# Kernel optimization log

Hardware: AMD Instinct MI355X
Metric: run time of the kernel (lower is better)

The kernel has to match this reference:

```python
import jax, jax.numpy as jnp
import numpy as np
from jax import lax

B, T, F, D, K = 64, 1000, 140, 256, 7
TAU, V_TH, EPS, ALPHA = 2.0, 1.0, 1e-5, 2.0
PAD = (K - 1) // 2

# Heaviside spike with ATan surrogate gradient (spikingjelly default, alpha=2)
@jax.custom_vjp
def spike_fn(x):
    return (x >= 0.0).astype(x.dtype)

def _spike_fwd(x):
    return spike_fn(x), x

def _spike_bwd(x, g):
    sg = (ALPHA / 2.0) / (1.0 + (jnp.pi / 2.0 * ALPHA * x) ** 2)
    return (g * sg,)

spike_fn.defvjp(_spike_fwd, _spike_bwd)

def lif(x_seq):
    """Multi-step LIF: v += (x - v)/tau, hard reset to 0 on spike. x_seq: (T,B,D)."""
    def step(v, x):
        v = v + (x - v) / TAU
        s = spike_fn(v - V_TH)
        return v * (1.0 - s), s
    _, spikes = lax.scan(step, jnp.zeros_like(x_seq[0]), x_seq)
    return spikes

def bn(x, g, b, m, v):
    # eval-mode BatchNorm1d over channel dim D (last axis of (T,B,D))
    return (x - m) * (g * lax.rsqrt(v + EPS)) + b

def setup_inputs() -> dict:
    key = jax.random.key(0)
    ks = jax.random.split(key, 4)
    s = 0.05
    return {
        "x": jax.random.normal(ks[0], (B, T, F), jnp.float32),
        "pw_w": jax.random.normal(ks[1], (D, F), jnp.float32) * s,
        "pw_b": jnp.zeros((D,), jnp.float32),
        "dw_w": jax.random.normal(ks[2], (D, 1, K), jnp.float32) * s,  # depthwise (O,I/g,K)
        "bn1_g": jnp.ones((D,), jnp.float32),
        "bn1_b": jnp.zeros((D,), jnp.float32),
        "bn1_m": jnp.zeros((D,), jnp.float32),
        "bn1_v": jnp.ones((D,), jnp.float32),
        "lin_w": jax.random.normal(ks[3], (D, D), jnp.float32) * s,
        "bn2_g": jnp.ones((D,), jnp.float32),
        "bn2_b": jnp.zeros((D,), jnp.float32),
        "bn2_m": jnp.zeros((D,), jnp.float32),
        "bn2_v": jnp.ones((D,), jnp.float32),
    }

def reference(x, pw_w, pw_b, dw_w, bn1_g, bn1_b, bn1_m, bn1_v,
              lin_w, bn2_g, bn2_b, bn2_m, bn2_v):
    # pointwise conv: (B,T,F) -> (B,D,T)
    h = jnp.einsum('btf,df->bdt', x, pw_w) + pw_b[None, :, None]
    # depthwise temporal conv, groups=D, same padding
    h = lax.conv_general_dilated(h, dw_w, window_strides=(1,),
                                 padding=[(PAD, PAD)], feature_group_count=D,
                                 dimension_numbers=('NCH', 'OIH', 'NCH'))
    h = jnp.transpose(h, (2, 0, 1))  # (T,B,D) multi-step layout
    h = lif(bn(h, bn1_g, bn1_b, bn1_m, bn1_v))
    residual = h
    h = jnp.einsum('tbd,ed->tbe', h, lin_w)
    h = lif(bn(h, bn2_g, bn2_b, bn2_m, bn2_v))
    return h + residual
```

## Files before the change

kernel.cpp:

```cpp
#include <hip/hip_runtime.h>
#include <hip/hip_bf16.h>

#define B_  64
#define T_  1000
#define F_  140
#define D_  256
#define EPS_ 1e-5f

#define W2_ 16

#define CL_ 50
#define NC_ 20

#define CWR_ 42
#define NCH_ 24
#define HST_ 268
#define AST_ 168

typedef __attribute__((ext_vector_type(8))) short bf16x8;
typedef __attribute__((ext_vector_type(4))) short bf16x4;
typedef __attribute__((ext_vector_type(4))) float f32x4;
typedef unsigned long long u64;

static __device__ inline short f2bf(float f) {
  __hip_bfloat16 h = __float2bfloat16(f);
  return *reinterpret_cast<short*>(&h);
}
static __device__ inline float bf2f(short s) {
  unsigned int u = ((unsigned int)(unsigned short)s) << 16;
  return __uint_as_float(u);
}

__global__ __launch_bounds__(256) void k0_prep(const float* __restrict__ lw,
                                               float* __restrict__ lwT,
                                               const float* __restrict__ pw,
                                               short* __restrict__ wfrag) {
  int i = blockIdx.x * 256 + threadIdx.x;
  if (i < 65536) {
    int e = i >> 8, d = i & 255;
    lwT[(size_t)d * D_ + e] = lw[(size_t)e * D_ + d];
  } else if (i < 65536 + 40960) {
    int j = i - 65536;
    int q = j & 7;
    int lane = (j >> 3) & 63;
    int rest = j >> 9;
    int kk = rest % 5, ntile = rest / 5;
    int n = ntile * 16 + (lane & 15);
    int k = kk * 32 + (lane >> 4) * 8 + q;
    wfrag[j] = (k < F_) ? f2bf(pw[(size_t)n * F_ + k]) : (short)0;
  }
}

__global__ __launch_bounds__(256, 4) void k12_fused(const float* __restrict__ x,
                                                    const short* __restrict__ wfrag,
                                                    const float* __restrict__ bias,
                                                    const float* __restrict__ dww,
                                                    const float* __restrict__ g1,
                                                    const float* __restrict__ b1,
                                                    const float* __restrict__ m1,
                                                    const float* __restrict__ v1,
                                                    u64* __restrict__ bits) {
  __shared__ short smem[64 * HST_];
  short* Abuf = smem;
  short* hbuf = smem;
  const int b = blockIdx.x;
  const int c = blockIdx.y;
  const int tb = CWR_ * c - 19;
  const int tid = threadIdx.x;
  const int lane = tid & 63, wv = tid >> 6;
  const int lr = lane & 15, quad = lane >> 4;

  {
    const int arow = tid >> 2, aseg = tid & 3;
    const int ak0 = aseg * 36;
    const int anum4 = (aseg == 3) ? 8 : 9;
    const int ta = tb + arow;
    short* adst = Abuf + arow * AST_ + ak0;
    if (ta >= 0 && ta < T_) {
      const float* xrow = x + ((size_t)b * T_ + ta) * F_ + ak0;
#pragma unroll
      for (int q = 0; q < 9; q++) {
        if (q < anum4) {
          float4 av = *(const float4*)(xrow + q * 4);
          bf16x4 pk = {f2bf(av.x), f2bf(av.y), f2bf(av.z), f2bf(av.w)};
          *(bf16x4*)(adst + q * 4) = pk;
        }
      }
    } else {
      bf16x4 z = {0, 0, 0, 0};
#pragma unroll
      for (int q = 0; q < 9; q++)
        if (q < anum4) *(bf16x4*)(adst + q * 4) = z;
    }
    if (aseg == 3) {
      bf16x4 z = {0, 0, 0, 0};
#pragma unroll
      for (int q = 0; q < 5; q++) *(bf16x4*)(adst + 32 + q * 4) = z;
    }
  }

  const short* wfb = wfrag + (size_t)(wv * 4 * 5) * 512 + lane * 8;
  bf16x8 bfr[4];
#pragma unroll
  for (int j = 0; j < 4; j++)
    bfr[j] = *(const bf16x8*)(wfb + (size_t)(j * 5 + 0) * 512);
  __syncthreads();

  f32x4 acc[4][4] = {};
#pragma unroll
  for (int kk = 0; kk < 5; kk++) {
    bf16x8 bnext[4];
    if (kk < 4) {
#pragma unroll
      for (int j = 0; j < 4; j++)
        bnext[j] = *(const bf16x8*)(wfb + (size_t)(j * 5 + kk + 1) * 512);
    }
    bf16x8 af[4];
#pragma unroll
    for (int i = 0; i < 4; i++)
      af[i] = *(const bf16x8*)(Abuf + (i * 16 + lr) * AST_ + kk * 32 + quad * 8);
#pragma unroll
    for (int i = 0; i < 4; i++)
#pragma unroll
      for (int j = 0; j < 4; j++)
        acc[i][j] = __builtin_amdgcn_mfma_f32_16x16x32_bf16(af[i], bfr[j], acc[i][j], 0, 0, 0);
    if (kk < 4) {
#pragma unroll
      for (int j = 0; j < 4; j++) bfr[j] = bnext[j];
    }
  }
  __syncthreads();

#pragma unroll
  for (int j = 0; j < 4; j++) {
    const int n = wv * 64 + j * 16 + lr;
    const float badd = bias[n];
#pragma unroll
    for (int i = 0; i < 4; i++) {
#pragma unroll
      for (int r = 0; r < 4; r++) {
        const int row = i * 16 + quad * 4 + r;
        const int t = tb + row;
        short val = (t >= 0 && t < T_) ? f2bf(acc[i][j][r] + badd) : (short)0;
        hbuf[row * HST_ + n] = val;
      }
    }
  }
  __syncthreads();

  {
    const int d = tid;
    const float scv = g1[d] * rsqrtf(v1[d] + EPS_);
    float w2[7];
#pragma unroll
    for (int k = 0; k < 7; k++) w2[k] = dww[d * 7 + k] * (0.5f * scv);
    const float sh2 = 0.5f * (b1[d] - m1[d] * scv);

    float win0 = bf2f(hbuf[0 * HST_ + d]);
    float win1 = bf2f(hbuf[1 * HST_ + d]);
    float win2 = bf2f(hbuf[2 * HST_ + d]);
    float win3 = bf2f(hbuf[3 * HST_ + d]);
    float win4 = bf2f(hbuf[4 * HST_ + d]);
    float win5 = bf2f(hbuf[5 * HST_ + d]);
    float v = 0.f;
    u64 mymask = 0;

#pragma unroll
    for (int s0 = 0; s0 < 56; s0 += 8) {
      float tap[8];
#pragma unroll
      for (int g = 0; g < 8; g++) tap[g] = bf2f(hbuf[(s0 + g + 6) * HST_ + d]);
#pragma unroll
      for (int g = 0; g < 8; g++) {
        const int s = s0 + g;
        float u2 = win0 * w2[0] + win1 * w2[1] + win2 * w2[2] + win3 * w2[3] +
                   win4 * w2[4] + win5 * w2[5] + tap[g] * w2[6] + sh2;
        v = 0.5f * v + u2;
        bool sp = (v >= 1.0f);
        if (s >= W2_) {
          u64 mask = __ballot(sp);
          if (lane == (s - W2_)) mymask = mask;
        }
        v = sp ? 0.f : v;
        win0 = win1; win1 = win2; win2 = win3; win3 = win4; win4 = win5; win5 = tap[g];
      }
    }
    {
      float tap[2];
#pragma unroll
      for (int g = 0; g < 2; g++) tap[g] = bf2f(hbuf[(56 + g + 6) * HST_ + d]);
#pragma unroll
      for (int g = 0; g < 2; g++) {
        const int s = 56 + g;
        float u2 = win0 * w2[0] + win1 * w2[1] + win2 * w2[2] + win3 * w2[3] +
                   win4 * w2[4] + win5 * w2[5] + tap[g] * w2[6] + sh2;
        v = 0.5f * v + u2;
        bool sp = (v >= 1.0f);
        u64 mask = __ballot(sp);
        if (lane == (s - W2_)) mymask = mask;
        v = sp ? 0.f : v;
        win0 = win1; win1 = win2; win2 = win3; win3 = win4; win4 = win5; win5 = tap[g];
      }
    }
    const int tw0 = CWR_ * c;
    if (lane < CWR_) {
      const int t = tw0 + lane;
      if (t < T_)
        bits[((size_t)b * 4 + wv) * T_ + t] = mymask;
    }
  }
}

__global__ __launch_bounds__(256) void k3_lin_lif(const u64* __restrict__ bits,
                                                  const float* __restrict__ lwT,
                                                  const float* __restrict__ g2,
                                                  const float* __restrict__ b2,
                                                  const float* __restrict__ m2,
                                                  const float* __restrict__ v2,
                                                  float* __restrict__ out) {
  __shared__ u64 sb[4 * 80];
  const int b = blockIdx.x;
  const int t0 = blockIdx.y * CL_;
  const int tstart = (t0 >= W2_) ? t0 - W2_ : 0;
  const int nwarm = t0 - tstart;
  const int nsteps = nwarm + CL_;
  const int e = threadIdx.x;
  {
    const int dq = e >> 6, sidx = e & 63;
    const u64* src = bits + ((size_t)b * 4 + dq) * T_ + tstart;
    if (sidx < nsteps) sb[dq * 80 + sidx] = src[sidx];
    const int s2 = sidx + 64;
    if (s2 < nsteps) sb[dq * 80 + s2] = src[s2];
  }
  __syncthreads();

  const float sc = g2[e] * rsqrtf(v2[e] + EPS_);
  const float shf = b2[e] - m2[e] * sc;
  const int eq = e >> 6, eb = e & 63;
  float v = 0.f;

  if (nwarm) {
#pragma unroll
    for (int s0 = 0; s0 < W2_; s0 += 4) {
      u64 a0[4], a1[4], a2[4], a3[4];
#pragma unroll
      for (int g = 0; g < 4; g++) {
        a0[g] = sb[0 * 80 + s0 + g]; a1[g] = sb[1 * 80 + s0 + g];
        a2[g] = sb[2 * 80 + s0 + g]; a3[g] = sb[3 * 80 + s0 + g];
      }
#pragma unroll
      for (int g = 0; g < 4; g++) {
        float u = shf;
        if (a0[g] | a1[g] | a2[g] | a3[g]) {
          float acc = 0.f;
          u64 mm;
          mm = a0[g]; while (mm) { int l = __builtin_ctzll(mm); mm &= mm - 1; acc += lwT[(size_t)(l) * D_ + e]; }
          mm = a1[g]; while (mm) { int l = __builtin_ctzll(mm); mm &= mm - 1; acc += lwT[(size_t)(64 + l) * D_ + e]; }
          mm = a2[g]; while (mm) { int l = __builtin_ctzll(mm); mm &= mm - 1; acc += lwT[(size_t)(128 + l) * D_ + e]; }
          mm = a3[g]; while (mm) { int l = __builtin_ctzll(mm); mm &= mm - 1; acc += lwT[(size_t)(192 + l) * D_ + e]; }
          u = acc * sc + shf;
        }
        v = 0.5f * (v + u);
        v = (v >= 1.0f) ? 0.f : v;
      }
    }
  }
  float* op = out + ((size_t)t0 * B_ + b) * D_ + e;
  const size_t ts = (size_t)B_ * D_;
#pragma unroll
  for (int s0 = 0; s0 < CL_; s0 += 5) {
    u64 a0[5], a1[5], a2[5], a3[5];
#pragma unroll
    for (int g = 0; g < 5; g++) {
      const int s = nwarm + s0 + g;
      a0[g] = sb[0 * 80 + s]; a1[g] = sb[1 * 80 + s];
      a2[g] = sb[2 * 80 + s]; a3[g] = sb[3 * 80 + s];
    }
#pragma unroll
    for (int g = 0; g < 5; g++) {
      float u = shf;
      if (a0[g] | a1[g] | a2[g] | a3[g]) {
        float acc = 0.f;
        u64 mm;
        mm = a0[g]; while (mm) { int l = __builtin_ctzll(mm); mm &= mm - 1; acc += lwT[(size_t)(l) * D_ + e]; }
        mm = a1[g]; while (mm) { int l = __builtin_ctzll(mm); mm &= mm - 1; acc += lwT[(size_t)(64 + l) * D_ + e]; }
        mm = a2[g]; while (mm) { int l = __builtin_ctzll(mm); mm &= mm - 1; acc += lwT[(size_t)(128 + l) * D_ + e]; }
        mm = a3[g]; while (mm) { int l = __builtin_ctzll(mm); mm &= mm - 1; acc += lwT[(size_t)(192 + l) * D_ + e]; }
        u = acc * sc + shf;
      }
      v = 0.5f * (v + u);
      bool sp = (v >= 1.0f);
      u64 myw = (eq == 0) ? a0[g] : (eq == 1) ? a1[g] : (eq == 2) ? a2[g] : a3[g];
      float s1 = (float)((myw >> eb) & 1ull);
      op[(size_t)(s0 + g) * ts] = (sp ? 1.0f : 0.0f) + s1;
      v = sp ? 0.f : v;
    }
  }
}

extern "C" void kernel_launch(void* const* d_in, const int* in_sizes, int n_in,
                              void* d_out, int out_size, void* d_ws, size_t ws_size,
                              hipStream_t stream) {
  const float* x    = (const float*)d_in[0];
  const float* pw_w = (const float*)d_in[1];
  const float* pw_b = (const float*)d_in[2];
  const float* dw_w = (const float*)d_in[3];
  const float* g1   = (const float*)d_in[4];
  const float* b1   = (const float*)d_in[5];
  const float* m1   = (const float*)d_in[6];
  const float* v1   = (const float*)d_in[7];
  const float* lw   = (const float*)d_in[8];
  const float* g2   = (const float*)d_in[9];
  const float* b2   = (const float*)d_in[10];
  const float* m2   = (const float*)d_in[11];
  const float* v2   = (const float*)d_in[12];
  float* out = (float*)d_out;

  char* ws = (char*)d_ws;
  u64* bits = (u64*)ws;
  float* lwT = (float*)(ws + 2048000);
  short* wfrag = (short*)(ws + 2048000 + 262144);

  k0_prep<<<(65536 + 40960 + 255) / 256, 256, 0, stream>>>(lw, lwT, pw_w, wfrag);
  dim3 g_k12(B_, NCH_);
  k12_fused<<<g_k12, 256, 0, stream>>>(x, wfrag, pw_b, dw_w, g1, b1, m1, v1, bits);
  dim3 g_k3(B_, NC_);
  k3_lin_lif<<<g_k3, 256, 0, stream>>>(bits, lwT, g2, b2, m2, v2, out);
}
```

Before: 156.2 us.

## Fuse sparse linear+LIF2 stage into conv/LIF1 kernel via shared-memory spike masks

Merges the second-stage kernel (sparse spike-driven linear, BN2, LIF2, residual output) into the first fused kernel. Spike ballot masks for all 58 steps of each chunk, warm-up included, are kept in shared memory rather than written to a global bit buffer and re-read. The second LIF is warmed up over the 16 overlap steps already present in each chunk. This removes one kernel launch and the global round trip of the spike bits. In exchange the fused kernel's blocks run longer and have more register and shared-memory pressure, and the time-chunking of stage two now follows the 42-step conv chunks.

```diff
diff --git a/kernel.cpp b/kernel.cpp
--- a/kernel.cpp
+++ b/kernel.cpp
@@ -7,13 +7,9 @@
 #define D_  256
 #define EPS_ 1e-5f
 
-#define W2_ 16
-
-#define CL_ 50
-#define NC_ 20
-
 #define CWR_ 42
 #define NCH_ 24
+#define W1_  16
 #define HST_ 268
 #define AST_ 168
 
@@ -51,16 +47,22 @@
   }
 }
 
-__global__ __launch_bounds__(256, 4) void k12_fused(const float* __restrict__ x,
-                                                    const short* __restrict__ wfrag,
-                                                    const float* __restrict__ bias,
-                                                    const float* __restrict__ dww,
-                                                    const float* __restrict__ g1,
-                                                    const float* __restrict__ b1,
-                                                    const float* __restrict__ m1,
-                                                    const float* __restrict__ v1,
-                                                    u64* __restrict__ bits) {
+__global__ __launch_bounds__(256, 4) void k123_fused(const float* __restrict__ x,
+                                                     const short* __restrict__ wfrag,
+                                                     const float* __restrict__ bias,
+                                                     const float* __restrict__ dww,
+                                                     const float* __restrict__ g1,
+                                                     const float* __restrict__ b1,
+                                                     const float* __restrict__ m1,
+                                                     const float* __restrict__ v1,
+                                                     const float* __restrict__ lwT,
+                                                     const float* __restrict__ g2,
+                                                     const float* __restrict__ b2,
+                                                     const float* __restrict__ m2,
+                                                     const float* __restrict__ v2,
+                                                     float* __restrict__ out) {
   __shared__ short smem[64 * HST_];
+  __shared__ u64 sbm[4 * 64];
   short* Abuf = smem;
   short* hbuf = smem;
   const int b = blockIdx.x;
@@ -177,10 +179,8 @@
                    win4 * w2[4] + win5 * w2[5] + tap[g] * w2[6] + sh2;
         v = 0.5f * v + u2;
         bool sp = (v >= 1.0f);
-        if (s >= W2_) {
-          u64 mask = __ballot(sp);
-          if (lane == (s - W2_)) mymask = mask;
-        }
+        u64 mask = __ballot(sp);
+        if (lane == s) mymask = mask;
         v = sp ? 0.f : v;
         win0 = win1; win1 = win2; win2 = win3; win3 = win4; win4 = win5; win5 = tap[g];
       }
@@ -197,103 +197,81 @@
         v = 0.5f * v + u2;
         bool sp = (v >= 1.0f);
         u64 mask = __ballot(sp);
-        if (lane == (s - W2_)) mymask = mask;
+        if (lane == s) mymask = mask;
         v = sp ? 0.f : v;
         win0 = win1; win1 = win2; win2 = win3; win3 = win4; win4 = win5; win5 = tap[g];
       }
     }
-    const int tw0 = CWR_ * c;
-    if (lane < CWR_) {
-      const int t = tw0 + lane;
-      if (t < T_)
-        bits[((size_t)b * 4 + wv) * T_ + t] = mymask;
-    }
-  }
-}
-
-__global__ __launch_bounds__(256) void k3_lin_lif(const u64* __restrict__ bits,
-                                                  const float* __restrict__ lwT,
-                                                  const float* __restrict__ g2,
-                                                  const float* __restrict__ b2,
-                                                  const float* __restrict__ m2,
-                                                  const float* __restrict__ v2,
-                                                  float* __restrict__ out) {
-  __shared__ u64 sb[4 * 80];
-  const int b = blockIdx.x;
-  const int t0 = blockIdx.y * CL_;
-  const int tstart = (t0 >= W2_) ? t0 - W2_ : 0;
-  const int nwarm = t0 - tstart;
-  const int nsteps = nwarm + CL_;
-  const int e = threadIdx.x;
+    if (lane < 58) sbm[wv * 64 + lane] = mymask;
+  }
+  __syncthreads();
+
   {
-    const int dq = e >> 6, sidx = e & 63;
-    const u64* src = bits + ((size_t)b * 4 + dq) * T_ + tstart;
-    if (sidx < nsteps) sb[dq * 80 + sidx] = src[sidx];
-    const int s2 = sidx + 64;
-    if (s2 < nsteps) sb[dq * 80 + s2] = src[s2];
-  }
-  __syncthreads();
-
-  const float sc = g2[e] * rsqrtf(v2[e] + EPS_);
-  const float shf = b2[e] - m2[e] * sc;
-  const int eq = e >> 6, eb = e & 63;
-  float v = 0.f;
-
-  if (nwarm) {
-#pragma unroll
-    for (int s0 = 0; s0 < W2_; s0 += 4) {
+    const int e = tid;
+    const float sc = g2[e] * rsqrtf(v2[e] + EPS_);
+    const float shf = b2[e] - m2[e] * sc;
+    const int eq = e >> 6, eb = e & 63;
+    float v = 0.f;
+
+#pragma unroll
+    for (int j0 = 0; j0 < W1_; j0 += 4) {
       u64 a0[4], a1[4], a2[4], a3[4];
 #pragma unroll
       for (int g = 0; g < 4; g++) {
-        a0[g] = sb[0 * 80 + s0 + g]; a1[g] = sb[1 * 80 + s0 + g];
-        a2[g] = sb[2 * 80 + s0 + g]; a3[g] = sb[3 * 80 + s0 + g];
+        a0[g] = sbm[0 * 64 + j0 + g]; a1[g] = sbm[1 * 64 + j0 + g];
+        a2[g] = sbm[2 * 64 + j0 + g]; a3[g] = sbm[3 * 64 + j0 + g];
       }
 #pragma unroll
       for (int g = 0; g < 4; g++) {
         float u = shf;
         if (a0[g] | a1[g] | a2[g] | a3[g]) {
-          float acc = 0.f;
+          float acc2 = 0.f;
           u64 mm;
-          mm = a0[g]; while (mm) { int l = __builtin_ctzll(mm); mm &= mm - 1; acc += lwT[(size_t)(l) * D_ + e]; }
-          mm = a1[g]; while (mm) { int l = __builtin_ctzll(mm); mm &= mm - 1; acc += lwT[(size_t)(64 + l) * D_ + e]; }
-          mm = a2[g]; while (mm) { int l = __builtin_ctzll(mm); mm &= mm - 1; acc += lwT[(size_t)(128 + l) * D_ + e]; }
-          mm = a3[g]; while (mm) { int l = __builtin_ctzll(mm); mm &= mm - 1; acc += lwT[(size_t)(192 + l) * D_ + e]; }
-          u = acc * sc + shf;
+          mm = a0[g]; while (mm) { int l = __builtin_ctzll(mm); mm &= mm - 1; acc2 += lwT[(size_t)(l) * D_ + e]; }
+          mm = a1[g]; while (mm) { int l = __builtin_ctzll(mm); mm &= mm - 1; acc2 += lwT[(size_t)(64 + l) * D_ + e]; }
+          mm = a2[g]; while (mm) { int l = __builtin_ctzll(mm); mm &= mm - 1; acc2 += lwT[(size_t)(128 + l) * D_ + e]; }
+          mm = a3[g]; while (mm) { int l = __builtin_ctzll(mm); mm &= mm - 1; acc2 += lwT[(size_t)(192 + l) * D_ + e]; }
+          u = acc2 * sc + shf;
         }
         v = 0.5f * (v + u);
         v = (v >= 1.0f) ? 0.f : v;
       }
     }
-  }
-  float* op = out + ((size_t)t0 * B_ + b) * D_ + e;
-  const size_t ts = (size_t)B_ * D_;
-#pragma unroll
-  for (int s0 = 0; s0 < CL_; s0 += 5) {
-    u64 a0[5], a1[5], a2[5], a3[5];
-#pragma unroll
-    for (int g = 0; g < 5; g++) {
-      const int s = nwarm + s0 + g;
-      a0[g] = sb[0 * 80 + s]; a1[g] = sb[1 * 80 + s];
-      a2[g] = sb[2 * 80 + s]; a3[g] = sb[3 * 80 + s];
-    }
-#pragma unroll
-    for (int g = 0; g < 5; g++) {
-      float u = shf;
-      if (a0[g] | a1[g] | a2[g] | a3[g]) {
-        float acc = 0.f;
-        u64 mm;
-        mm = a0[g]; while (mm) { int l = __builtin_ctzll(mm); mm &= mm - 1; acc += lwT[(size_t)(l) * D_ + e]; }
-        mm = a1[g]; while (mm) { int l = __builtin_ctzll(mm); mm &= mm - 1; acc += lwT[(size_t)(64 + l) * D_ + e]; }
-        mm = a2[g]; while (mm) { int l = __builtin_ctzll(mm); mm &= mm - 1; acc += lwT[(size_t)(128 + l) * D_ + e]; }
-        mm = a3[g]; while (mm) { int l = __builtin_ctzll(mm); mm &= mm - 1; acc += lwT[(size_t)(192 + l) * D_ + e]; }
-        u = acc * sc + shf;
-      }
-      v = 0.5f * (v + u);
-      bool sp = (v >= 1.0f);
-      u64 myw = (eq == 0) ? a0[g] : (eq == 1) ? a1[g] : (eq == 2) ? a2[g] : a3[g];
-      float s1 = (float)((myw >> eb) & 1ull);
-      op[(size_t)(s0 + g) * ts] = (sp ? 1.0f : 0.0f) + s1;
-      v = sp ? 0.f : v;
+    const int tw0 = CWR_ * c;
+    const int smax = T_ - tw0;
+    float* op = out + ((size_t)tw0 * B_ + b) * D_ + e;
+    const size_t ts = (size_t)B_ * D_;
+#pragma unroll
+    for (int i0 = 0; i0 < CWR_; i0 += 6) {
+      u64 a0[6], a1[6], a2[6], a3[6];
+#pragma unroll
+      for (int g = 0; g < 6; g++) {
+        const int j = W1_ + i0 + g;
+        a0[g] = sbm[0 * 64 + j]; a1[g] = sbm[1 * 64 + j];
+        a2[g] = sbm[2 * 64 + j]; a3[g] = sbm[3 * 64 + j];
+      }
+#pragma unroll
+      for (int g = 0; g < 6; g++) {
+        float u = shf;
+        if (a0[g] | a1[g] | a2[g] | a3[g]) {
+          float acc2 = 0.f;
+          u64 mm;
+          mm = a0[g]; while (mm) { int l = __builtin_ctzll(mm); mm &= mm - 1; acc2 += lwT[(size_t)(l) * D_ + e]; }
+          mm = a1[g]; while (mm) { int l = __builtin_ctzll(mm); mm &= mm - 1; acc2 += lwT[(size_t)(64 + l) * D_ + e]; }
+          mm = a2[g]; while (mm) { int l = __builtin_ctzll(mm); mm &= mm - 1; acc2 += lwT[(size_t)(128 + l) * D_ + e]; }
+          mm = a3[g]; while (mm) { int l = __builtin_ctzll(mm); mm &= mm - 1; acc2 += lwT[(size_t)(192 + l) * D_ + e]; }
+          u = acc2 * sc + shf;
+        }
+        v = 0.5f * (v + u);
+        bool sp = (v >= 1.0f);
+        const int i = i0 + g;
+        if (i < smax) {
+          u64 myw = (eq == 0) ? a0[g] : (eq == 1) ? a1[g] : (eq == 2) ? a2[g] : a3[g];
+          float s1 = (float)((myw >> eb) & 1ull);
+          op[(size_t)i * ts] = (sp ? 1.0f : 0.0f) + s1;
+        }
+        v = sp ? 0.f : v;
+      }
     }
   }
 }
@@ -317,13 +295,11 @@
   float* out = (float*)d_out;
 
   char* ws = (char*)d_ws;
-  u64* bits = (u64*)ws;
-  float* lwT = (float*)(ws + 2048000);
-  short* wfrag = (short*)(ws + 2048000 + 262144);
+  float* lwT = (float*)ws;
+  short* wfrag = (short*)(ws + 262144);
 
   k0_prep<<<(65536 + 40960 + 255) / 256, 256, 0, stream>>>(lw, lwT, pw_w, wfrag);
-  dim3 g_k12(B_, NCH_);
-  k12_fused<<<g_k12, 256, 0, stream>>>(x, wfrag, pw_b, dw_w, g1, b1, m1, v1, bits);
-  dim3 g_k3(B_, NC_);
-  k3_lin_lif<<<g_k3, 256, 0, stream>>>(bits, lwT, g2, b2, m2, v2, out);
-}
+  dim3 g_k123(B_, NCH_);
+  k123_fused<<<g_k123, 256, 0, stream>>>(x, wfrag, pw_b, dw_w, g1, b1, m1, v1,
+                                         lwT, g2, b2, m2, v2, out);
+}
```

Result: faster. 152.9 us (-2.1%).
